# Performance work log

Hardware: AMD Instinct MI355X
Metric: run time of the kernel (lower is better)

## Reference

```python
import jax, jax.numpy as jnp
import numpy as np
from jax import lax

FAN_IN = 16          # fixed number of parents per decoder node
THRESHOLD = 12       # node is active iff >= 12/16 parents are active
K_NODES = 1024       # decoders in this layer
M_PREV = 1024        # nodes in previous layer
N_SPATIAL = 64       # n x n output matrices


def setup_inputs() -> dict:
    key = jax.random.key(0)
    k1, k2, k3, k4, k5 = jax.random.split(key, 5)
    prev_outputs = jax.random.normal(k1, (M_PREV, N_SPATIAL, N_SPATIAL), dtype=jnp.float32)
    # Bernoulli(0.85) so the 12/16 threshold gate is genuinely data-dependent
    prev_is_active = jax.random.bernoulli(k2, 0.85, (M_PREV,))
    parent_indices = jax.random.randint(k3, (K_NODES, FAN_IN), 0, M_PREV, dtype=jnp.int32)
    # Per-node decoder params: 3x3 conv collapsing 16 parent channels -> 1 map, plus bias
    W = jax.random.normal(k4, (K_NODES, FAN_IN, 3, 3), dtype=jnp.float32) * 0.05
    b = jax.random.normal(k5, (K_NODES,), dtype=jnp.float32) * 0.05
    return {"prev_outputs": prev_outputs, "prev_is_active": prev_is_active,
            "parent_indices": parent_indices, "W": W, "b": b}


def reference(prev_outputs, prev_is_active, parent_indices, W, b):
    K, n = parent_indices.shape[0], prev_outputs.shape[-1]
    # Irregular static-wiring gather: (K, 16, n, n) and (K, 16)
    gathered = prev_outputs[parent_indices]
    gathered_flags = prev_is_active[parent_indices]
    # Threshold gate: node active iff >= 12 of its 16 parents are active
    out_active = jnp.sum(gathered_flags.astype(jnp.int32), axis=1) >= THRESHOLD  # (K,)
    # K independent 16->1 convs with distinct weights == one grouped conv (groups = K)
    x = gathered.reshape(1, K * FAN_IN, n, n)          # NCHW
    y = lax.conv_general_dilated(
        x, W, window_strides=(1, 1), padding='SAME',
        dimension_numbers=('NCHW', 'OIHW', 'NCHW'),
        feature_group_count=K,
    )[0]                                               # (K, n, n)
    y = jnp.tanh(y + b[:, None, None])
    # Inactive nodes emit a zero tensor
    out = jnp.where(out_active[:, None, None], y, jnp.zeros((), dtype=y.dtype))
    return out, out_active
```

## Files before the change

kernel.cpp:

```cpp
#include <hip/hip_runtime.h>

#define KN      1024
#define FAN_IN  16
#define NSP     64
#define THRESH  12

__device__ __forceinline__ float tanh_fast(float x) {
    float ax = fabsf(x);
    float e  = __expf(-2.0f * ax);
    float r  = 1.0f - 2.0f * e * __builtin_amdgcn_rcpf(1.0f + e);
    return copysignf(r, x);
}

__device__ __forceinline__ float2 fma2(float w, float2 v, float2 a) {
    a.x = fmaf(w, v.x, a.x);
    a.y = fmaf(w, v.y, a.y);
    return a;
}

__global__ __launch_bounds__(256) void decoder_kernel(
    const float* __restrict__ prev_outputs,
    const void*  __restrict__ prev_is_active,
    const int*   __restrict__ parent_indices,
    const float* __restrict__ Wt,
    const float* __restrict__ bias,
    float*       __restrict__ out)
{
    const int bid  = blockIdx.x;
    const int k    = bid >> 1;
    const int half = bid & 1;
    const int tid  = threadIdx.x;
    const int col  = tid & 63;
    const int rg   = tid >> 6;
    const int r0   = half * 32 + rg * 8;

    bool bytemode = false;
    {
        const unsigned* sv = (const unsigned*)prev_is_active;
        #pragma unroll
        for (int i = 0; i < 16; ++i)
            if (sv[i] > 1u) bytemode = true;
    }

    int cnt = 0;
    #pragma unroll
    for (int i = 0; i < FAN_IN; ++i) {
        int p = parent_indices[k * FAN_IN + i];
        int f;
        if (bytemode) f = (((const unsigned char*)prev_is_active)[p] != 0);
        else          f = (((const int*)prev_is_active)[p] != 0);
        cnt += f;
    }
    const bool active = (cnt >= THRESH);

    const size_t obase = (size_t)k * (NSP * NSP);
    if (half == 0 && tid == 0)
        out[(size_t)KN * NSP * NSP + k] = active ? 1.0f : 0.0f;

    if (!active) {
        float4 z = make_float4(0.f, 0.f, 0.f, 0.f);
        float4* o4 = (float4*)(out + obase + (size_t)half * 32 * NSP);
        #pragma unroll
        for (int i = tid; i < 32 * NSP / 4; i += 256) o4[i] = z;
        return;
    }

    float2 accs[4];
    #pragma unroll
    for (int s = 0; s < 4; ++s) accs[s] = make_float2(0.f, 0.f);

    const int  idxC = r0 * NSP + col;
    const bool rlo  = (r0 > 0);
    const bool rhi  = (r0 < 56);
    const bool cl   = (col > 0);
    const bool cr   = (col < 63);

    for (int c = 0; c < FAN_IN; ++c) {
        const int p = parent_indices[k * FAN_IN + c];
        const float* __restrict__ src = prev_outputs + (size_t)p * (NSP * NSP);
        const float* wc = Wt + ((size_t)k * FAN_IN + c) * 9;
        const float w00 = wc[0], w01 = wc[1], w02 = wc[2];
        const float w10 = wc[3], w11 = wc[4], w12 = wc[5];
        const float w20 = wc[6], w21 = wc[7], w22 = wc[8];

        float2 L[6], C[6], R[6];

        C[0].x = rlo ? src[idxC - NSP] : 0.0f;
        #pragma unroll
        for (int j = 1; j <= 5; ++j) C[j].x = src[idxC + (j - 1) * NSP];
        #pragma unroll
        for (int j = 0; j <= 4; ++j) C[j].y = src[idxC + (j + 3) * NSP];
        C[5].y = rhi ? src[idxC + 8 * NSP] : 0.0f;

        if (cl) {
            L[0].x = rlo ? src[idxC - 1 - NSP] : 0.0f;
            #pragma unroll
            for (int j = 1; j <= 5; ++j) L[j].x = src[idxC - 1 + (j - 1) * NSP];
            #pragma unroll
            for (int j = 0; j <= 4; ++j) L[j].y = src[idxC - 1 + (j + 3) * NSP];
            L[5].y = rhi ? src[idxC - 1 + 8 * NSP] : 0.0f;
        } else {
            #pragma unroll
            for (int j = 0; j < 6; ++j) L[j] = make_float2(0.f, 0.f);
        }

        if (cr) {
            R[0].x = rlo ? src[idxC + 1 - NSP] : 0.0f;
            #pragma unroll
            for (int j = 1; j <= 5; ++j) R[j].x = src[idxC + 1 + (j - 1) * NSP];
            #pragma unroll
            for (int j = 0; j <= 4; ++j) R[j].y = src[idxC + 1 + (j + 3) * NSP];
            R[5].y = rhi ? src[idxC + 1 + 8 * NSP] : 0.0f;
        } else {
            #pragma unroll
            for (int j = 0; j < 6; ++j) R[j] = make_float2(0.f, 0.f);
        }

        #pragma unroll
        for (int s = 0; s < 4; ++s) {
            float2 a = accs[s];
            a = fma2(w00, L[s],     a);
            a = fma2(w01, C[s],     a);
            a = fma2(w02, R[s],     a);
            a = fma2(w10, L[s + 1], a);
            a = fma2(w11, C[s + 1], a);
            a = fma2(w12, R[s + 1], a);
            a = fma2(w20, L[s + 2], a);
            a = fma2(w21, C[s + 2], a);
            a = fma2(w22, R[s + 2], a);
            accs[s] = a;
        }
    }

    const float bk = bias[k];
    #pragma unroll
    for (int s = 0; s < 4; ++s) {
        out[obase + (size_t)(r0 + s)     * NSP + col] = tanh_fast(accs[s].x + bk);
        out[obase + (size_t)(r0 + 4 + s) * NSP + col] = tanh_fast(accs[s].y + bk);
    }
}

extern "C" void kernel_launch(void* const* d_in, const int* in_sizes, int n_in,
                              void* d_out, int out_size, void* d_ws, size_t ws_size,
                              hipStream_t stream) {
    const float* prev_outputs   = (const float*)d_in[0];
    const void*  prev_is_active = d_in[1];
    const int*   parent_indices = (const int*)d_in[2];
    const float* Wt             = (const float*)d_in[3];
    const float* bias           = (const float*)d_in[4];
    float*       out            = (float*)d_out;

    decoder_kernel<<<dim3(KN * 2), dim3(256), 0, stream>>>(
        prev_outputs, prev_is_active, parent_indices, Wt, bias, out);
}
```

Before: 42.48 us.

## Tile each node's conv as 4x4 outputs per thread with float4 loads

Each block now handles one whole node (1024 blocks) instead of half a node. Each thread computes a 4x4 output tile, loading six rows as float4 plus two scalar halo values, and writes float4 stores. The aim is fewer load instructions per output and better vectorised global access than the earlier 8-row by 1-column scheme. In exchange the grid has half as many blocks, and it relies on clamped-row loads with mask multiplies.

After: 73.16 us. 1.72x slower.

```diff
diff --git a/kernel.cpp b/kernel.cpp
--- a/kernel.cpp
+++ b/kernel.cpp
@@ -12,12 +12,6 @@
     return copysignf(r, x);
 }
 
-__device__ __forceinline__ float2 fma2(float w, float2 v, float2 a) {
-    a.x = fmaf(w, v.x, a.x);
-    a.y = fmaf(w, v.y, a.y);
-    return a;
-}
-
 __global__ __launch_bounds__(256) void decoder_kernel(
     const float* __restrict__ prev_outputs,
     const void*  __restrict__ prev_is_active,
@@ -26,13 +20,12 @@
     const float* __restrict__ bias,
     float*       __restrict__ out)
 {
-    const int bid  = blockIdx.x;
-    const int k    = bid >> 1;
-    const int half = bid & 1;
-    const int tid  = threadIdx.x;
-    const int col  = tid & 63;
-    const int rg   = tid >> 6;
-    const int r0   = half * 32 + rg * 8;
+    const int k   = blockIdx.x;
+    const int tid = threadIdx.x;
+    const int cg  = tid & 15;
+    const int rg  = tid >> 4;
+    const int c0  = cg * 4;
+    const int r0  = rg * 4;
 
     bool bytemode = false;
     {
@@ -54,89 +47,75 @@
     const bool active = (cnt >= THRESH);
 
     const size_t obase = (size_t)k * (NSP * NSP);
-    if (half == 0 && tid == 0)
+    if (tid == 0)
         out[(size_t)KN * NSP * NSP + k] = active ? 1.0f : 0.0f;
 
     if (!active) {
         float4 z = make_float4(0.f, 0.f, 0.f, 0.f);
-        float4* o4 = (float4*)(out + obase + (size_t)half * 32 * NSP);
+        float4* o4 = (float4*)(out + obase);
         #pragma unroll
-        for (int i = tid; i < 32 * NSP / 4; i += 256) o4[i] = z;
+        for (int i = tid; i < NSP * NSP / 4; i += 256) o4[i] = z;
         return;
     }
 
-    float2 accs[4];
+    const float mL = (cg > 0)  ? 1.0f : 0.0f;
+    const float mR = (cg < 15) ? 1.0f : 0.0f;
+    const float mT = (rg > 0)  ? 1.0f : 0.0f;
+    const float mB = (rg < 15) ? 1.0f : 0.0f;
+    const int   cL = (cg > 0)  ? c0 - 1 : 0;
+    const int   cR = (cg < 15) ? c0 + 4 : 63;
+
+    float acc[4][4];
     #pragma unroll
-    for (int s = 0; s < 4; ++s) accs[s] = make_float2(0.f, 0.f);
+    for (int r = 0; r < 4; ++r)
+        #pragma unroll
+        for (int c = 0; c < 4; ++c) acc[r][c] = 0.0f;
 
-    const int  idxC = r0 * NSP + col;
-    const bool rlo  = (r0 > 0);
-    const bool rhi  = (r0 < 56);
-    const bool cl   = (col > 0);
-    const bool cr   = (col < 63);
-
-    for (int c = 0; c < FAN_IN; ++c) {
-        const int p = parent_indices[k * FAN_IN + c];
+    for (int ch = 0; ch < FAN_IN; ++ch) {
+        const int p = parent_indices[k * FAN_IN + ch];
         const float* __restrict__ src = prev_outputs + (size_t)p * (NSP * NSP);
-        const float* wc = Wt + ((size_t)k * FAN_IN + c) * 9;
-        const float w00 = wc[0], w01 = wc[1], w02 = wc[2];
-        const float w10 = wc[3], w11 = wc[4], w12 = wc[5];
-        const float w20 = wc[6], w21 = wc[7], w22 = wc[8];
-
-        float2 L[6], C[6], R[6];
-
-        C[0].x = rlo ? src[idxC - NSP] : 0.0f;
+        const float* wc = Wt + ((size_t)k * FAN_IN + ch) * 9;
+        float w[9];
         #pragma unroll
-        for (int j = 1; j <= 5; ++j) C[j].x = src[idxC + (j - 1) * NSP];
-        #pragma unroll
-        for (int j = 0; j <= 4; ++j) C[j].y = src[idxC + (j + 3) * NSP];
-        C[5].y = rhi ? src[idxC + 8 * NSP] : 0.0f;
-
-        if (cl) {
-            L[0].x = rlo ? src[idxC - 1 - NSP] : 0.0f;
-            #pragma unroll
-            for (int j = 1; j <= 5; ++j) L[j].x = src[idxC - 1 + (j - 1) * NSP];
-            #pragma unroll
-            for (int j = 0; j <= 4; ++j) L[j].y = src[idxC - 1 + (j + 3) * NSP];
-            L[5].y = rhi ? src[idxC - 1 + 8 * NSP] : 0.0f;
-        } else {
-            #pragma unroll
-            for (int j = 0; j < 6; ++j) L[j] = make_float2(0.f, 0.f);
-        }
-
-        if (cr) {
-            R[0].x = rlo ? src[idxC + 1 - NSP] : 0.0f;
-            #pragma unroll
-            for (int j = 1; j <= 5; ++j) R[j].x = src[idxC + 1 + (j - 1) * NSP];
-            #pragma unroll
-            for (int j = 0; j <= 4; ++j) R[j].y = src[idxC + 1 + (j + 3) * NSP];
-            R[5].y = rhi ? src[idxC + 1 + 8 * NSP] : 0.0f;
-        } else {
-            #pragma unroll
-            for (int j = 0; j < 6; ++j) R[j] = make_float2(0.f, 0.f);
-        }
+        for (int i = 0; i < 9; ++i) w[i] = wc[i];
 
         #pragma unroll
-        for (int s = 0; s < 4; ++s) {
-            float2 a = accs[s];
-            a = fma2(w00, L[s],     a);
-            a = fma2(w01, C[s],     a);
-            a = fma2(w02, R[s],     a);
-            a = fma2(w10, L[s + 1], a);
-            a = fma2(w11, C[s + 1], a);
-            a = fma2(w12, R[s + 1], a);
-            a = fma2(w20, L[s + 2], a);
-            a = fma2(w21, C[s + 2], a);
-            a = fma2(w22, R[s + 2], a);
-            accs[s] = a;
+        for (int j = 0; j < 6; ++j) {
+            int gr = r0 - 1 + j;
+            gr = (gr < 0) ? 0 : (gr > 63 ? 63 : gr);
+            const float* rp = src + gr * NSP;
+
+            float4 m  = *(const float4*)(rp + c0);
+            float  l  = rp[cL] * mL;
+            float  r_ = rp[cR] * mR;
+
+            if (j == 0) { m.x *= mT; m.y *= mT; m.z *= mT; m.w *= mT; l *= mT; r_ *= mT; }
+            if (j == 5) { m.x *= mB; m.y *= mB; m.z *= mB; m.w *= mB; l *= mB; r_ *= mB; }
+
+            const int rlo = (j >= 2) ? (j - 2) : 0;
+            const int rhi = (j <= 3) ? j : 3;
+            #pragma unroll
+            for (int r = rlo; r <= rhi; ++r) {
+                const float w0 = w[(j - r) * 3 + 0];
+                const float w1 = w[(j - r) * 3 + 1];
+                const float w2 = w[(j - r) * 3 + 2];
+                acc[r][0] = fmaf(w0, l,   fmaf(w1, m.x, fmaf(w2, m.y, acc[r][0])));
+                acc[r][1] = fmaf(w0, m.x, fmaf(w1, m.y, fmaf(w2, m.z, acc[r][1])));
+                acc[r][2] = fmaf(w0, m.y, fmaf(w1, m.z, fmaf(w2, m.w, acc[r][2])));
+                acc[r][3] = fmaf(w0, m.z, fmaf(w1, m.w, fmaf(w2, r_,  acc[r][3])));
+            }
         }
     }
 
     const float bk = bias[k];
     #pragma unroll
-    for (int s = 0; s < 4; ++s) {
-        out[obase + (size_t)(r0 + s)     * NSP + col] = tanh_fast(accs[s].x + bk);
-        out[obase + (size_t)(r0 + 4 + s) * NSP + col] = tanh_fast(accs[s].y + bk);
+    for (int r = 0; r < 4; ++r) {
+        float4 o;
+        o.x = tanh_fast(acc[r][0] + bk);
+        o.y = tanh_fast(acc[r][1] + bk);
+        o.z = tanh_fast(acc[r][2] + bk);
+        o.w = tanh_fast(acc[r][3] + bk);
+        *(float4*)(out + obase + (size_t)(r0 + r) * NSP + c0) = o;
     }
 }
 
@@ -150,6 +129,6 @@
     const float* bias           = (const float*)d_in[4];
     float*       out            = (float*)d_out;
 
-    decoder_kernel<<<dim3(KN * 2), dim3(256), 0, stream>>>(
+    decoder_kernel<<<dim3(KN), dim3(256), 0, stream>>>(
         prev_outputs, prev_is_active, parent_indices, Wt, bias, out);
 }
```
